# Kernel tuning notes

Measured on AMD Instinct MI355X. Metric: run time of the kernel, lower is better.

The kernel has to match this reference:

```python
import jax, jax.numpy as jnp
import numpy as np

B, N, D, H = 4, 4096, 512, 512
EDGE_P = 0.01  # adjacency density


def _glorot(key, shape):
    fan_in, fan_out = shape
    limit = np.sqrt(6.0 / (fan_in + fan_out)).astype(np.float32)
    return jax.random.uniform(key, shape, jnp.float32, -limit, limit)


def setup_inputs() -> dict:
    key = jax.random.key(0)
    ks = jax.random.split(key, 9)
    batch_graph = jax.random.normal(ks[0], (B, N, D), jnp.float32)
    adj = (jax.random.uniform(ks[1], (B, N, N)) < EDGE_P).astype(jnp.float32)
    adj = jnp.minimum(adj + jnp.eye(N, dtype=jnp.float32)[None], 1.0)  # self loops, 0/1
    return {
        "batch_graph": batch_graph,
        "adj": adj,
        "W1": _glorot(ks[2], (D, H)), "b1": jnp.zeros((H,), jnp.float32),
        "W2": _glorot(ks[3], (H, H)), "b2": jnp.zeros((H,), jnp.float32),
        "W3": _glorot(ks[4], (H, D)), "b3": jnp.zeros((D,), jnp.float32),
    }


def _normalize_adj(adj):
    # Faithful to GCN.normalize_sparse_adj: D^{-1/2} A^T D^{-1/2}
    rowsum = adj.sum(axis=1)                       # [B, N] (sum over dim 1, as in torch)
    d_inv_sqrt = jnp.where(rowsum > 0, jax.lax.rsqrt(jnp.maximum(rowsum, 1e-30)), 0.0)
    # (A @ diag(d))^T @ diag(d)  ->  d_i * A[j,i] * d_j
    return d_inv_sqrt[:, :, None] * jnp.swapaxes(adj, 1, 2) * d_inv_sqrt[:, None, :]


def reference(batch_graph, adj, W1, b1, W2, b2, W3, b3):
    # Block-diagonal big_adj @ big_graph == independent per-batch matmuls;
    # we exploit that instead of materializing the [B*N, B*N] dense matrix.
    a = _normalize_adj(adj)                                   # [B, N, N]
    # GraphConvolution (pygcn-style): out = adj @ (x @ W) + b; dropout = identity (eval)
    h = jax.nn.relu(jnp.einsum('bij,bjd->bid', a, batch_graph @ W1) + b1)
    h = jax.nn.relu(jnp.einsum('bij,bjd->bid', a, h @ W2) + b2)
    out = jnp.einsum('bij,bjd->bid', a, h @ W3) + b3          # [B, N, D]
    return out
```

## Files before the change

kernel.cpp:

```cpp
#include <hip/hip_runtime.h>
#include <stdint.h>

#define CAP 128
#define RPB 4

typedef __attribute__((ext_vector_type(8))) short bf16x8;
typedef __attribute__((ext_vector_type(4))) float f32x4;
typedef __attribute__((ext_vector_type(4))) uint32_t u32x4;

typedef __attribute__((address_space(3))) uint32_t lds_u32;
typedef __attribute__((address_space(1))) const uint32_t glb_u32;

__device__ __forceinline__ unsigned short f2bf(float f) {
  union { float f; uint32_t u; } c; c.f = f;
  return (unsigned short)((c.u + 0x7fffu + ((c.u >> 16) & 1u)) >> 16);
}
__device__ __forceinline__ float bf2f(uint32_t b) {
  union { uint32_t u; float f; } c; c.u = b << 16; return c.f;
}
__device__ __forceinline__ float as_f32(uint32_t u) {
  union { uint32_t u; float f; } c; c.u = u; return c.f;
}

__global__ __launch_bounds__(256) void k_init(const uint32_t* __restrict__ a,
                                              int* __restrict__ cnt,
                                              int* __restrict__ flag) {
  __shared__ int sfound;
  int t = threadIdx.x;
  if (t == 0) sfound = 0;
  bool found = false;
  for (int i = t; i < 16384; i += 256) {
    cnt[i] = 0;
    uint32_t x = a[i];
    if (x == 0x00003F80u || x == 0x3F803F80u) found = true;
  }
  __syncthreads();
  if (found) sfound = 1;
  __syncthreads();
  if (t == 0) flag[0] = sfound;
}

__global__ __launch_bounds__(256) void k_stage(const void* __restrict__ adjp,
                                               int* __restrict__ cnt,
                                               int* __restrict__ cols,
                                               const void* __restrict__ xp,
                                               ushort* __restrict__ xb,
                                               const void* w1, const void* w2,
                                               const void* w3,
                                               ushort* __restrict__ wt1,
                                               ushort* __restrict__ wt2,
                                               ushort* __restrict__ wt3,
                                               const int* __restrict__ flag) {
  __shared__ uint32_t lw[64][65];
  int bid = blockIdx.x;
  int tid = threadIdx.x;
  int flagv = flag[0];

  if (bid < 2048) {
    if (flagv) {
      const uint4* a = (const uint4*)adjp;
      for (int gid = bid * 256 + tid; gid < 8388608; gid += 524288) {
        uint4 v = a[gid];
        int i0 = (gid & 511) * 8;
        int j  = (gid >> 9) & 4095;
        int b  = gid >> 21;
        int base = b << 12;
        uint32_t w[4] = {v.x, v.y, v.z, v.w};
#pragma unroll
        for (int q = 0; q < 4; q++) {
          if (w[q] & 0xffffu) {
            int c = base + i0 + q * 2;
            int p = atomicAdd(&cnt[c], 1);
            if (p < CAP) cols[(size_t)c * CAP + p] = j;
          }
          if (w[q] >> 16) {
            int c = base + i0 + q * 2 + 1;
            int p = atomicAdd(&cnt[c], 1);
            if (p < CAP) cols[(size_t)c * CAP + p] = j;
          }
        }
      }
    } else {
      const float4* a = (const float4*)adjp;
      for (int v4 = bid * 256 + tid; v4 < 16777216; v4 += 524288) {
        float4 v = a[v4];
        int i0 = (v4 & 1023) * 4;
        int j  = (v4 >> 10) & 4095;
        int b  = v4 >> 22;
        int base = b << 12;
        float e[4] = {v.x, v.y, v.z, v.w};
#pragma unroll
        for (int q = 0; q < 4; q++) {
          if (e[q] != 0.0f) {
            int c = base + i0 + q;
            int p = atomicAdd(&cnt[c], 1);
            if (p < CAP) cols[(size_t)c * CAP + p] = j;
          }
        }
      }
    }
  } else if (bid < 2560) {
    if (flagv) {
      const uint4* in = (const uint4*)xp;
      for (int gid = (bid - 2048) * 256 + tid; gid < 1048576; gid += 131072)
        ((uint4*)xb)[gid] = in[gid];
    } else {
      const float4* in = (const float4*)xp;
      for (int gid = (bid - 2048) * 256 + tid; gid < 1048576; gid += 131072) {
#pragma unroll
        for (int it = 0; it < 2; it++) {
          int i = gid + it * 1048576;
          float4 v = in[i];
          uint32_t lo = (uint32_t)f2bf(v.x) | ((uint32_t)f2bf(v.y) << 16);
          uint32_t hi = (uint32_t)f2bf(v.z) | ((uint32_t)f2bf(v.w) << 16);
          ((uint2*)xb)[i] = make_uint2(lo, hi);
        }
      }
    }
  } else {
    int wi = bid - 2560;
    int w = wi >> 6;
    int tile = wi & 63;
    int tm = tile >> 3, tn = tile & 7;
    const void* wp = (w == 0) ? w1 : (w == 1) ? w2 : w3;
    ushort* wt = (w == 0) ? wt1 : (w == 1) ? wt2 : wt3;
    int tx = tid & 63, ty = tid >> 6;
    if (flagv) {
      const ushort* ws = (const ushort*)wp;
#pragma unroll
      for (int s = 0; s < 64; s += 4) {
        int row = s + ty;
        lw[row][tx] = ws[(size_t)(tm * 64 + row) * 512 + tn * 64 + tx];
      }
    } else {
      const float* ws = (const float*)wp;
#pragma unroll
      for (int s = 0; s < 64; s += 4) {
        int row = s + ty;
        lw[row][tx] = __float_as_uint(ws[(size_t)(tm * 64 + row) * 512 + tn * 64 + tx]);
      }
    }
    __syncthreads();
#pragma unroll
    for (int s = 0; s < 64; s += 4) {
      int row = s + ty;
      uint32_t bits = lw[tx][row];
      ushort o = flagv ? (ushort)bits : f2bf(__uint_as_float(bits));
      wt[(size_t)(tn * 64 + row) * 512 + tm * 64 + tx] = o;
    }
  }
}

__device__ __forceinline__ void gl_lds16(const ushort* g, ushort* l) {
  __builtin_amdgcn_global_load_lds((glb_u32*)g, (lds_u32*)l, 16, 0, 0);
}

__global__ __launch_bounds__(256) void k_gemm(const ushort* __restrict__ X,
                                              const ushort* __restrict__ WT,
                                              ushort* __restrict__ Z) {
  __shared__ ushort As[128 * 32];
  __shared__ ushort Bs[128 * 32];
  const int K = 512, NO = 512;
  int tid = threadIdx.x;
  int m0 = blockIdx.y * 128, n0 = blockIdx.x * 128;
  int lane = tid & 63;
  int wv = tid >> 6;
  int wm = (wv >> 1) << 6;
  int wn = (wv & 1) << 6;
  int lr = lane & 15;
  int lq = lane >> 4;

  f32x4 zero = {0.f, 0.f, 0.f, 0.f};
  f32x4 acc[4][4];
#pragma unroll
  for (int im = 0; im < 4; im++)
#pragma unroll
    for (int in_ = 0; in_ < 4; in_++) acc[im][in_] = zero;

  const ushort* Xg = X  + (size_t)(m0 + (tid >> 2)) * K + ((tid & 3) << 3);
  const ushort* Wg = WT + (size_t)(n0 + (tid >> 2)) * K + ((tid & 3) << 3);

  for (int kt = 0; kt < K; kt += 32) {
    __syncthreads();
    gl_lds16(Xg + kt,                    &As[tid * 8]);
    gl_lds16(Xg + kt + (size_t)64 * K,   &As[2048 + tid * 8]);
    gl_lds16(Wg + kt,                    &Bs[tid * 8]);
    gl_lds16(Wg + kt + (size_t)64 * K,   &Bs[2048 + tid * 8]);
    __syncthreads();
    bf16x8 af[4], bfr[4];
#pragma unroll
    for (int im = 0; im < 4; im++)
      af[im] = *(const bf16x8*)&As[(wm + im * 16 + lr) * 32 + lq * 8];
#pragma unroll
    for (int in_ = 0; in_ < 4; in_++)
      bfr[in_] = *(const bf16x8*)&Bs[(wn + in_ * 16 + lr) * 32 + lq * 8];
#pragma unroll
    for (int im = 0; im < 4; im++)
#pragma unroll
      for (int in_ = 0; in_ < 4; in_++)
        acc[im][in_] = __builtin_amdgcn_mfma_f32_16x16x32_bf16(
            af[im], bfr[in_], acc[im][in_], 0, 0, 0);
  }

#pragma unroll
  for (int im = 0; im < 4; im++) {
    int row0 = m0 + wm + im * 16 + lq * 4;
#pragma unroll
    for (int in_ = 0; in_ < 4; in_++) {
      int col = n0 + wn + in_ * 16 + lr;
#pragma unroll
      for (int r = 0; r < 4; r++)
        Z[(size_t)(row0 + r) * NO + col] = f2bf(acc[im][in_][r]);
    }
  }
}

__global__ __launch_bounds__(256) void k_spmm(const ushort* __restrict__ Z,
                                              const int* __restrict__ cnt,
                                              const int* __restrict__ cols,
                                              const void* __restrict__ bias,
                                              void* __restrict__ outp,
                                              int do_relu, int is_final,
                                              const int* __restrict__ flag) {
  __shared__ int   sj[RPB][CAP];
  __shared__ float sv[RPB][CAP];
  int B = blockIdx.x;
  int wv = threadIdx.x >> 6;
  int lane = threadIdx.x & 63;
  int batch = (B & 7) >> 1;
  int lb = ((B >> 3) << 1) | (B & 1);
  int r = (batch << 12) + lb * RPB + wv;
  int base = batch << 12;

  int cr = cnt[r];
  float dr = (cr > 0) ? 1.0f / sqrtf((float)cr) : 0.0f;
  int nnz = (cr > CAP) ? CAP : cr;
  for (int k = lane; k < nnz; k += 64) {
    int j = __builtin_nontemporal_load(&cols[(size_t)r * CAP + k]);
    int cj = cnt[base + j];
    sj[wv][k] = j;
    sv[wv][k] = dr * ((cj > 0) ? 1.0f / sqrtf((float)cj) : 0.0f);
  }

  const ushort* Zb = Z + (size_t)base * 512 + lane * 8;
  float a[8];
  if (flag[0]) {
    uint4 bb = *((const uint4*)bias + lane);
    uint32_t w[4] = {bb.x, bb.y, bb.z, bb.w};
#pragma unroll
    for (int q = 0; q < 4; q++) {
      a[q * 2]     = bf2f(w[q] & 0xffffu);
      a[q * 2 + 1] = bf2f(w[q] >> 16);
    }
  } else {
    const float4* bp = (const float4*)bias + lane * 2;
    float4 bb0 = bp[0], bb1 = bp[1];
    a[0] = bb0.x; a[1] = bb0.y; a[2] = bb0.z; a[3] = bb0.w;
    a[4] = bb1.x; a[5] = bb1.y; a[6] = bb1.z; a[7] = bb1.w;
  }

  int k = 0;
  for (; k + 2 <= nnz; k += 2) {
    int j0 = sj[wv][k], j1 = sj[wv][k + 1];
    float v0 = sv[wv][k], v1 = sv[wv][k + 1];
    uint4 z0 = *(const uint4*)(Zb + (size_t)j0 * 512);
    uint4 z1 = *(const uint4*)(Zb + (size_t)j1 * 512);
    uint32_t w0[4] = {z0.x, z0.y, z0.z, z0.w};
    uint32_t w1[4] = {z1.x, z1.y, z1.z, z1.w};
#pragma unroll
    for (int q = 0; q < 4; q++) {
      a[q * 2]     += v0 * as_f32(w0[q] << 16);
      a[q * 2 + 1] += v0 * as_f32(w0[q] & 0xffff0000u);
      a[q * 2]     += v1 * as_f32(w1[q] << 16);
      a[q * 2 + 1] += v1 * as_f32(w1[q] & 0xffff0000u);
    }
  }
  if (k < nnz) {
    int j0 = sj[wv][k];
    float v0 = sv[wv][k];
    uint4 z0 = *(const uint4*)(Zb + (size_t)j0 * 512);
    uint32_t w0[4] = {z0.x, z0.y, z0.z, z0.w};
#pragma unroll
    for (int q = 0; q < 4; q++) {
      a[q * 2]     += v0 * as_f32(w0[q] << 16);
      a[q * 2 + 1] += v0 * as_f32(w0[q] & 0xffff0000u);
    }
  }

  if (do_relu) {
#pragma unroll
    for (int q = 0; q < 8; q++) a[q] = fmaxf(a[q], 0.f);
  }

  if (!is_final || flag[0]) {
    u32x4 o;
    o[0] = (uint32_t)f2bf(a[0]) | ((uint32_t)f2bf(a[1]) << 16);
    o[1] = (uint32_t)f2bf(a[2]) | ((uint32_t)f2bf(a[3]) << 16);
    o[2] = (uint32_t)f2bf(a[4]) | ((uint32_t)f2bf(a[5]) << 16);
    o[3] = (uint32_t)f2bf(a[6]) | ((uint32_t)f2bf(a[7]) << 16);
    __builtin_nontemporal_store(
        o, (u32x4*)((ushort*)outp + (size_t)r * 512 + lane * 8));
  } else {
    f32x4 o0 = {a[0], a[1], a[2], a[3]};
    f32x4 o1 = {a[4], a[5], a[6], a[7]};
    f32x4* op = (f32x4*)((float*)outp + (size_t)r * 512 + lane * 8);
    __builtin_nontemporal_store(o0, op);
    __builtin_nontemporal_store(o1, op + 1);
  }
}

extern "C" void kernel_launch(void* const* d_in, const int* in_sizes, int n_in,
                              void* d_out, int out_size, void* d_ws, size_t ws_size,
                              hipStream_t stream) {
  const void* X  = d_in[0];
  const void* A  = d_in[1];
  const void* W1 = d_in[2]; const void* b1 = d_in[3];
  const void* W2 = d_in[4]; const void* b2 = d_in[5];
  const void* W3 = d_in[6]; const void* b3 = d_in[7];

  char* ws = (char*)d_ws;
  size_t off = 0;
  auto alloc = [&](size_t bytes) -> void* {
    void* p = ws + off;
    off += (bytes + 255) & ~(size_t)255;
    return p;
  };
  int*    cnt  = (int*)alloc(16384 * 4);
  int*    flag = (int*)alloc(4);
  int*    cols = (int*)alloc((size_t)16384 * CAP * 4);
  ushort* W1T  = (ushort*)alloc(512 * 512 * 2);
  ushort* W2T  = (ushort*)alloc(512 * 512 * 2);
  ushort* W3T  = (ushort*)alloc(512 * 512 * 2);
  ushort* Xb   = (ushort*)alloc((size_t)16384 * 512 * 2);
  ushort* Zb   = (ushort*)alloc((size_t)16384 * 512 * 2);
  ushort* Hb   = (ushort*)alloc((size_t)16384 * 512 * 2);

  k_init<<<1, 256, 0, stream>>>((const uint32_t*)A, cnt, flag);
  k_stage<<<2752, 256, 0, stream>>>(A, cnt, cols, X, Xb,
                                    W1, W2, W3, W1T, W2T, W3T, flag);

  dim3 gg(4, 128);
  k_gemm<<<gg, 256, 0, stream>>>(Xb, W1T, Zb);
  k_spmm<<<4096, 256, 0, stream>>>(Zb, cnt, cols, b1, Hb, 1, 0, flag);
  k_gemm<<<gg, 256, 0, stream>>>(Hb, W2T, Zb);
  k_spmm<<<4096, 256, 0, stream>>>(Zb, cnt, cols, b2, Xb, 1, 0, flag);
  k_gemm<<<gg, 256, 0, stream>>>(Xb, W3T, Zb);
  k_spmm<<<4096, 256, 0, stream>>>(Zb, cnt, cols, b3, d_out, 0, 1, flag);
}
```

Measured before the change: 602.0 us.

## Build adjacency column lists with per-segment slots instead of global atomics

Replaces the atomic-counter scatter that built each row's neighbour list with a scheme where every thread owns one output row and one 512-wide segment of the adjacency. The thread scans its segment, writes up to 28 indices into a private slot range, and stores a per-segment byte count. The SpMM kernel reads the eight counts with one 64-bit load, sums them with a multiply trick, and compacts the segments into shared memory. This removes the atomics, the count-zeroing pass and the contention on shared counters. In exchange it imposes a per-segment cap of 28, which can truncate unusually dense rows, and reads the adjacency in long per-thread strided loops.

```diff
diff --git a/kernel.cpp b/kernel.cpp
--- a/kernel.cpp
+++ b/kernel.cpp
@@ -1,8 +1,10 @@
 #include <hip/hip_runtime.h>
 #include <stdint.h>
 
-#define CAP 128
-#define RPB 4
+#define SLOTS 28
+#define SEGS  8
+#define CAPN  224
+#define RPB   4
 
 typedef __attribute__((ext_vector_type(8))) short bf16x8;
 typedef __attribute__((ext_vector_type(4))) float f32x4;
@@ -23,14 +25,12 @@
 }
 
 __global__ __launch_bounds__(256) void k_init(const uint32_t* __restrict__ a,
-                                              int* __restrict__ cnt,
                                               int* __restrict__ flag) {
   __shared__ int sfound;
   int t = threadIdx.x;
   if (t == 0) sfound = 0;
   bool found = false;
   for (int i = t; i < 16384; i += 256) {
-    cnt[i] = 0;
     uint32_t x = a[i];
     if (x == 0x00003F80u || x == 0x3F803F80u) found = true;
   }
@@ -41,7 +41,7 @@
 }
 
 __global__ __launch_bounds__(256) void k_stage(const void* __restrict__ adjp,
-                                               int* __restrict__ cnt,
+                                               uint8_t* __restrict__ scnt,
                                                int* __restrict__ cols,
                                                const void* __restrict__ xp,
                                                ushort* __restrict__ xb,
@@ -56,57 +56,50 @@
   int tid = threadIdx.x;
   int flagv = flag[0];
 
-  if (bid < 2048) {
+  if (bid < 512) {
+    int wid = tid >> 6, lane = tid & 63;
+    int t = bid * 4 + wid;
+    int b = t >> 9;
+    int rem = t & 511;
+    int g = rem >> 3;
+    int c = rem & 7;
+    int i = g * 64 + lane;
+    size_t r = ((size_t)b << 12) + i;
+    int* crow = cols + r * CAPN + c * SLOTS;
+    int p = 0;
+    int jb = c * 512;
     if (flagv) {
-      const uint4* a = (const uint4*)adjp;
-      for (int gid = bid * 256 + tid; gid < 8388608; gid += 524288) {
-        uint4 v = a[gid];
-        int i0 = (gid & 511) * 8;
-        int j  = (gid >> 9) & 4095;
-        int b  = gid >> 21;
-        int base = b << 12;
-        uint32_t w[4] = {v.x, v.y, v.z, v.w};
-#pragma unroll
-        for (int q = 0; q < 4; q++) {
-          if (w[q] & 0xffffu) {
-            int c = base + i0 + q * 2;
-            int p = atomicAdd(&cnt[c], 1);
-            if (p < CAP) cols[(size_t)c * CAP + p] = j;
-          }
-          if (w[q] >> 16) {
-            int c = base + i0 + q * 2 + 1;
-            int p = atomicAdd(&cnt[c], 1);
-            if (p < CAP) cols[(size_t)c * CAP + p] = j;
-          }
-        }
+      const ushort* cb = (const ushort*)adjp + ((size_t)b << 24) + i;
+      for (int j0 = 0; j0 < 512; j0 += 8) {
+        ushort v[8];
+#pragma unroll
+        for (int u = 0; u < 8; u++)
+          v[u] = cb[(size_t)(jb + j0 + u) << 12];
+#pragma unroll
+        for (int u = 0; u < 8; u++)
+          if (v[u]) { if (p < SLOTS) crow[p] = jb + j0 + u; p++; }
       }
     } else {
-      const float4* a = (const float4*)adjp;
-      for (int v4 = bid * 256 + tid; v4 < 16777216; v4 += 524288) {
-        float4 v = a[v4];
-        int i0 = (v4 & 1023) * 4;
-        int j  = (v4 >> 10) & 4095;
-        int b  = v4 >> 22;
-        int base = b << 12;
-        float e[4] = {v.x, v.y, v.z, v.w};
-#pragma unroll
-        for (int q = 0; q < 4; q++) {
-          if (e[q] != 0.0f) {
-            int c = base + i0 + q;
-            int p = atomicAdd(&cnt[c], 1);
-            if (p < CAP) cols[(size_t)c * CAP + p] = j;
-          }
-        }
-      }
-    }
-  } else if (bid < 2560) {
+      const float* cb = (const float*)adjp + ((size_t)b << 24) + i;
+      for (int j0 = 0; j0 < 512; j0 += 8) {
+        float v[8];
+#pragma unroll
+        for (int u = 0; u < 8; u++)
+          v[u] = cb[(size_t)(jb + j0 + u) << 12];
+#pragma unroll
+        for (int u = 0; u < 8; u++)
+          if (v[u] != 0.0f) { if (p < SLOTS) crow[p] = jb + j0 + u; p++; }
+      }
+    }
+    scnt[r * 8 + c] = (uint8_t)(p > SLOTS ? SLOTS : p);
+  } else if (bid < 1024) {
     if (flagv) {
       const uint4* in = (const uint4*)xp;
-      for (int gid = (bid - 2048) * 256 + tid; gid < 1048576; gid += 131072)
+      for (int gid = (bid - 512) * 256 + tid; gid < 1048576; gid += 131072)
         ((uint4*)xb)[gid] = in[gid];
     } else {
       const float4* in = (const float4*)xp;
-      for (int gid = (bid - 2048) * 256 + tid; gid < 1048576; gid += 131072) {
+      for (int gid = (bid - 512) * 256 + tid; gid < 1048576; gid += 131072) {
 #pragma unroll
         for (int it = 0; it < 2; it++) {
           int i = gid + it * 1048576;
@@ -118,7 +111,7 @@
       }
     }
   } else {
-    int wi = bid - 2560;
+    int wi = bid - 1024;
     int w = wi >> 6;
     int tile = wi & 63;
     int tm = tile >> 3, tn = tile & 7;
@@ -216,14 +209,14 @@
 }
 
 __global__ __launch_bounds__(256) void k_spmm(const ushort* __restrict__ Z,
-                                              const int* __restrict__ cnt,
+                                              const uint8_t* __restrict__ scnt,
                                               const int* __restrict__ cols,
                                               const void* __restrict__ bias,
                                               void* __restrict__ outp,
                                               int do_relu, int is_final,
                                               const int* __restrict__ flag) {
-  __shared__ int   sj[RPB][CAP];
-  __shared__ float sv[RPB][CAP];
+  __shared__ int   sj[RPB][CAPN];
+  __shared__ float sv[RPB][CAPN];
   int B = blockIdx.x;
   int wv = threadIdx.x >> 6;
   int lane = threadIdx.x & 63;
@@ -232,15 +225,24 @@
   int r = (batch << 12) + lb * RPB + wv;
   int base = batch << 12;
 
-  int cr = cnt[r];
+  uint64_t s8 = *(const uint64_t*)(scnt + (size_t)r * 8);
+  int cr = (int)((s8 * 0x0101010101010101ull) >> 56);
   float dr = (cr > 0) ? 1.0f / sqrtf((float)cr) : 0.0f;
-  int nnz = (cr > CAP) ? CAP : cr;
-  for (int k = lane; k < nnz; k += 64) {
-    int j = __builtin_nontemporal_load(&cols[(size_t)r * CAP + k]);
-    int cj = cnt[base + j];
-    sj[wv][k] = j;
-    sv[wv][k] = dr * ((cj > 0) ? 1.0f / sqrtf((float)cj) : 0.0f);
-  }
+  int run = 0;
+#pragma unroll
+  for (int s = 0; s < SEGS; s++) {
+    int sc = (int)((s8 >> (8 * s)) & 255);
+    if (lane < sc) {
+      int j = __builtin_nontemporal_load(
+          &cols[(size_t)r * CAPN + s * SLOTS + lane]);
+      uint64_t t8 = *(const uint64_t*)(scnt + ((size_t)(base + j)) * 8);
+      int cj = (int)((t8 * 0x0101010101010101ull) >> 56);
+      sj[wv][run + lane] = j;
+      sv[wv][run + lane] = dr * ((cj > 0) ? 1.0f / sqrtf((float)cj) : 0.0f);
+    }
+    run += sc;
+  }
+  int nnz = run;
 
   const ushort* Zb = Z + (size_t)base * 512 + lane * 8;
   float a[8];
@@ -325,25 +327,25 @@
     off += (bytes + 255) & ~(size_t)255;
     return p;
   };
-  int*    cnt  = (int*)alloc(16384 * 4);
-  int*    flag = (int*)alloc(4);
-  int*    cols = (int*)alloc((size_t)16384 * CAP * 4);
-  ushort* W1T  = (ushort*)alloc(512 * 512 * 2);
-  ushort* W2T  = (ushort*)alloc(512 * 512 * 2);
-  ushort* W3T  = (ushort*)alloc(512 * 512 * 2);
-  ushort* Xb   = (ushort*)alloc((size_t)16384 * 512 * 2);
-  ushort* Zb   = (ushort*)alloc((size_t)16384 * 512 * 2);
-  ushort* Hb   = (ushort*)alloc((size_t)16384 * 512 * 2);
-
-  k_init<<<1, 256, 0, stream>>>((const uint32_t*)A, cnt, flag);
-  k_stage<<<2752, 256, 0, stream>>>(A, cnt, cols, X, Xb,
+  uint8_t* scnt = (uint8_t*)alloc(16384 * 8);
+  int*     flag = (int*)alloc(4);
+  int*     cols = (int*)alloc((size_t)16384 * CAPN * 4);
+  ushort*  W1T  = (ushort*)alloc(512 * 512 * 2);
+  ushort*  W2T  = (ushort*)alloc(512 * 512 * 2);
+  ushort*  W3T  = (ushort*)alloc(512 * 512 * 2);
+  ushort*  Xb   = (ushort*)alloc((size_t)16384 * 512 * 2);
+  ushort*  Zb   = (ushort*)alloc((size_t)16384 * 512 * 2);
+  ushort*  Hb   = (ushort*)alloc((size_t)16384 * 512 * 2);
+
+  k_init<<<1, 256, 0, stream>>>((const uint32_t*)A, flag);
+  k_stage<<<1216, 256, 0, stream>>>(A, scnt, cols, X, Xb,
                                     W1, W2, W3, W1T, W2T, W3T, flag);
 
   dim3 gg(4, 128);
   k_gemm<<<gg, 256, 0, stream>>>(Xb, W1T, Zb);
-  k_spmm<<<4096, 256, 0, stream>>>(Zb, cnt, cols, b1, Hb, 1, 0, flag);
+  k_spmm<<<4096, 256, 0, stream>>>(Zb, scnt, cols, b1, Hb, 1, 0, flag);
   k_gemm<<<gg, 256, 0, stream>>>(Hb, W2T, Zb);
-  k_spmm<<<4096, 256, 0, stream>>>(Zb, cnt, cols, b2, Xb, 1, 0, flag);
+  k_spmm<<<4096, 256, 0, stream>>>(Zb, scnt, cols, b2, Xb, 1, 0, flag);
   k_gemm<<<gg, 256, 0, stream>>>(Xb, W3T, Zb);
-  k_spmm<<<4096, 256, 0, stream>>>(Zb, cnt, cols, b3, d_out, 0, 1, flag);
-}
+  k_spmm<<<4096, 256, 0, stream>>>(Zb, scnt, cols, b3, d_out, 0, 1, flag);
+}
```

Result: slower. 675.8 us (+12.3%).
